# Kernel optimization log

Hardware: AMD Instinct MI355X
Metric: run time of the kernel (lower is better)

Reference implementation:

```python
import jax, jax.numpy as jnp
import numpy as np
import math

D_MODEL, N_HEADS, D_K, D_C, D_HR = 1024, 8, 128, 32, 32
B, S = 4, 2048


def setup_inputs() -> dict:
    key = jax.random.key(0)
    ks = jax.random.split(key, 17)
    def lin(k, fan_in, fan_out):
        lim = 1.0 / math.sqrt(fan_in)
        kw, kb = jax.random.split(k)
        W = jax.random.uniform(kw, (fan_in, fan_out), jnp.float32, -lim, lim)
        b = jax.random.uniform(kb, (fan_out,), jnp.float32, -lim, lim)
        return W, b
    W_DQ, b_DQ = lin(ks[0], D_MODEL, D_C)
    W_UQ, b_UQ = lin(ks[1], D_C, N_HEADS * D_K)
    W_DKV, b_DKV = lin(ks[2], D_MODEL, D_C)
    W_UK, b_UK = lin(ks[3], D_C, N_HEADS * D_K)
    W_UV, b_UV = lin(ks[4], D_C, N_HEADS * D_K)
    W_QR, b_QR = lin(ks[5], D_C, N_HEADS * D_HR)
    W_KR, b_KR = lin(ks[6], D_MODEL, D_HR)
    W_O, b_O = lin(ks[7], N_HEADS * D_K, D_MODEL)
    h_t = jax.random.normal(ks[8], (B, S, D_MODEL), jnp.float32)
    return {"h_t": h_t,
            "W_DQ": W_DQ, "b_DQ": b_DQ, "W_UQ": W_UQ, "b_UQ": b_UQ,
            "W_DKV": W_DKV, "b_DKV": b_DKV, "W_UK": W_UK, "b_UK": b_UK,
            "W_UV": W_UV, "b_UV": b_UV, "W_QR": W_QR, "b_QR": b_QR,
            "W_KR": W_KR, "b_KR": b_KR, "W_O": W_O, "b_O": b_O}


def reference(h_t, W_DQ, b_DQ, W_UQ, b_UQ, W_DKV, b_DKV, W_UK, b_UK,
              W_UV, b_UV, W_QR, b_QR, W_KR, b_KR, W_O, b_O):
    b, s, _ = h_t.shape
    # low-rank latent projections
    c_q = h_t @ W_DQ + b_DQ                       # [B,S,d_c]
    c_kv = h_t @ W_DKV + b_DKV                    # [B,S,d_c]
    # content heads: [B,H,S,d_k]
    q_c = (c_q @ W_UQ + b_UQ).reshape(b, s, N_HEADS, D_K).transpose(0, 2, 1, 3)
    k_c = (c_kv @ W_UK + b_UK).reshape(b, s, N_HEADS, D_K).transpose(0, 2, 1, 3)
    v_c = (c_kv @ W_UV + b_UV).reshape(b, s, N_HEADS, D_K).transpose(0, 2, 1, 3)
    # rope sub-dims (apply_rope is identity in the source): [B,H,S,d_hR]
    q_r = (c_q @ W_QR + b_QR).reshape(b, s, N_HEADS, D_HR).transpose(0, 2, 1, 3)
    k_r = (h_t @ W_KR + b_KR)[:, None, :, :]      # [B,1,S,d_hR], shared across heads
    k_r = jnp.broadcast_to(k_r, (b, N_HEADS, s, D_HR))
    # concat content + rope dims
    q = jnp.concatenate([q_c, q_r], axis=-1)      # [B,H,S,d_k+d_hR]
    k = jnp.concatenate([k_c, k_r], axis=-1)
    scale = 1.0 / math.sqrt(D_K + D_HR)
    scores = jnp.einsum('bhsd,bhtd->bhst', q, k) * scale
    attn = jax.nn.softmax(scores, axis=-1)
    o = jnp.einsum('bhst,bhtd->bhsd', attn, v_c)  # [B,H,S,d_k]
    o = o.transpose(0, 2, 1, 3).reshape(b, s, N_HEADS * D_K)
    return o @ W_O + b_O
```

## Files before the change

kernel.cpp:

```cpp
#include <hip/hip_runtime.h>
#include <hip/hip_bf16.h>

#define B_SZ 4
#define S_SZ 2048
#define DM   1024
#define NH   8
#define DK   128
#define DC   32
#define DHR  32
#define DQK  160
#define T_TOK (B_SZ * S_SZ)
#define SCALE 0.07905694150420949f
#define C2LOG 0.11405506439f
#define NT    (S_SZ / 64)
#define NCOL  3328

typedef unsigned int uint;
typedef unsigned short ushort;
typedef __attribute__((ext_vector_type(8))) short short8;
typedef __attribute__((ext_vector_type(4))) float floatx4;
typedef __attribute__((ext_vector_type(16))) float floatx16;
typedef __attribute__((ext_vector_type(4))) uint uintx4;

__device__ __forceinline__ ushort f2bf(float f) {
    uint u = __float_as_uint(f);
    uint r = u + 0x7fffu + ((u >> 16) & 1u);
    return (ushort)(r >> 16);
}
__device__ __forceinline__ uint packbf(float x, float y) {
    return (uint)f2bf(x) | ((uint)f2bf(y) << 16);
}

__device__ __forceinline__ void glds16(const ushort* g, ushort* l) {
    __builtin_amdgcn_global_load_lds(
        (const __attribute__((address_space(1))) uint*)g,
        (__attribute__((address_space(3))) uint*)l, 16, 0, 0);
}

__global__ __launch_bounds__(256) void prep_kernel(
    const float* __restrict__ W_O,
    const float* __restrict__ W_UQ, const float* __restrict__ b_UQ,
    const float* __restrict__ W_QR, const float* __restrict__ b_QR,
    const float* __restrict__ W_UK, const float* __restrict__ b_UK,
    const float* __restrict__ W_UV, const float* __restrict__ b_UV,
    const float* __restrict__ W_DQ, const float* __restrict__ b_DQ,
    const float* __restrict__ W_DKV, const float* __restrict__ b_DKV,
    const float* __restrict__ W_KR, const float* __restrict__ b_KR,
    ushort* __restrict__ wot,
    ushort* __restrict__ wcat, float* __restrict__ bcat,
    ushort* __restrict__ wdcat, float* __restrict__ bdcat)
{
    __shared__ float t[32][33];
    const int bid = blockIdx.x;
    const int tx = threadIdx.x & 31, ty = threadIdx.x >> 5;

    if (bid < 1024) {
        const int n0 = (bid & 31) * 32, k0 = (bid >> 5) * 32;
        #pragma unroll
        for (int j = 0; j < 32; j += 8)
            t[ty + j][tx] = W_O[(size_t)(k0 + ty + j) * DM + n0 + tx];
        __syncthreads();
        #pragma unroll
        for (int j = 0; j < 32; j += 8)
            wot[(size_t)(n0 + ty + j) * DM + k0 + tx] = f2bf(t[tx][ty + j]);
    } else if (bid < 1128) {
        const int c0 = (bid - 1024) * 32;
        const float* W; const float* bias; int stride, sc0;
        if (c0 < 1024)      { W = W_UQ; bias = b_UQ; stride = 1024; sc0 = c0; }
        else if (c0 < 1280) { W = W_QR; bias = b_QR; stride = 256;  sc0 = c0 - 1024; }
        else if (c0 < 2304) { W = W_UK; bias = b_UK; stride = 1024; sc0 = c0 - 1280; }
        else                { W = W_UV; bias = b_UV; stride = 1024; sc0 = c0 - 2304; }
        #pragma unroll
        for (int j = 0; j < 4; ++j) {
            int k = ty + j * 8;
            t[k][tx] = W[(size_t)k * stride + sc0 + tx];
        }
        __syncthreads();
        #pragma unroll
        for (int j = 0; j < 4; ++j) {
            int cc = ty + j * 8;
            wcat[(size_t)(c0 + cc) * 32 + tx] = f2bf(t[tx][cc]);
        }
        if (threadIdx.x < 32) bcat[c0 + threadIdx.x] = bias[sc0 + threadIdx.x];
    } else {
        const int idx = bid - 1128;
        const int wsel = idx >> 5;
        const int k0 = (idx & 31) * 32;
        const float* W    = (wsel == 0) ? W_DQ  : (wsel == 1) ? W_DKV : W_KR;
        const float* bias = (wsel == 0) ? b_DQ  : (wsel == 1) ? b_DKV : b_KR;
        #pragma unroll
        for (int j = 0; j < 32; j += 8)
            t[ty + j][tx] = W[(size_t)(k0 + ty + j) * 32 + tx];
        __syncthreads();
        #pragma unroll
        for (int j = 0; j < 32; j += 8)
            wdcat[(size_t)(wsel * 32 + ty + j) * DM + k0 + tx] = f2bf(t[tx][ty + j]);
        if (k0 == 0 && threadIdx.x < 32)
            bdcat[wsel * 32 + threadIdx.x] = bias[threadIdx.x];
    }
}

__global__ __launch_bounds__(128) void latent_mfma_kernel(
    const float* __restrict__ h_t,
    const ushort* __restrict__ wdcat, const float* __restrict__ bdcat,
    ushort* __restrict__ cqbf, ushort* __restrict__ ckvbf, ushort* __restrict__ krbf)
{
    const int tid  = threadIdx.x;
    const int wave = tid >> 6;
    const int lane = tid & 63;
    const int quad = lane >> 4;
    const int l16  = lane & 15;

    const int tok = blockIdx.x * 32 + wave * 16 + l16;

    floatx4 acc[6];
    #pragma unroll
    for (int ct = 0; ct < 6; ++ct) acc[ct] = (floatx4){0.f, 0.f, 0.f, 0.f};

    const float* hrow = h_t + (size_t)tok * DM + quad * 8;

    #pragma unroll 2
    for (int k0 = 0; k0 < DM; k0 += 32) {
        float4 f0 = *(const float4*)&hrow[k0];
        float4 f1 = *(const float4*)&hrow[k0 + 4];
        uint b0, b1, b2, b3;
        asm("v_cvt_pk_bf16_f32 %0, %1, %2" : "=v"(b0) : "v"(f0.x), "v"(f0.y));
        asm("v_cvt_pk_bf16_f32 %0, %1, %2" : "=v"(b1) : "v"(f0.z), "v"(f0.w));
        asm("v_cvt_pk_bf16_f32 %0, %1, %2" : "=v"(b2) : "v"(f1.x), "v"(f1.y));
        asm("v_cvt_pk_bf16_f32 %0, %1, %2" : "=v"(b3) : "v"(f1.z), "v"(f1.w));
        short8 bf = __builtin_bit_cast(short8, (uintx4){b0, b1, b2, b3});
        #pragma unroll
        for (int ct = 0; ct < 6; ++ct) {
            short8 af = *(const short8*)&wdcat[(size_t)(ct * 16 + l16) * DM + k0 + quad * 8];
            acc[ct] = __builtin_amdgcn_mfma_f32_16x16x32_bf16(af, bf, acc[ct], 0, 0, 0);
        }
    }

    const int q4 = quad * 4;
    #pragma unroll
    for (int ct = 0; ct < 6; ++ct) {
        float4 b4 = *(const float4*)&bdcat[ct * 16 + q4];
        uint w0, w1;
        asm("v_cvt_pk_bf16_f32 %0, %1, %2" : "=v"(w0)
            : "v"(acc[ct][0] + b4.x), "v"(acc[ct][1] + b4.y));
        asm("v_cvt_pk_bf16_f32 %0, %1, %2" : "=v"(w1)
            : "v"(acc[ct][2] + b4.z), "v"(acc[ct][3] + b4.w));
        int col = ct * 16 + q4;
        ushort* outp = (col < 32) ? cqbf : (col < 64) ? ckvbf : krbf;
        int cc = col & 31;
        *(uint2*)&outp[(size_t)tok * 32 + cc] = make_uint2(w0, w1);
    }
}

__global__ __launch_bounds__(256) void build_qkv_mfma_kernel(
    const ushort* __restrict__ cqbf, const ushort* __restrict__ ckvbf,
    const ushort* __restrict__ krbf,
    const ushort* __restrict__ wcat, const float* __restrict__ bcat,
    ushort* __restrict__ q_ws, ushort* __restrict__ k_ws, ushort* __restrict__ v_ws)
{
    const int tid  = threadIdx.x;
    const int wave = tid >> 6;
    const int lane = tid & 63;
    const int quad = lane >> 4;
    const int l16  = lane & 15;

    const int tok = blockIdx.x * 64 + wave * 16 + l16;
    const int hp  = blockIdx.y;
    const int bb  = tok >> 11, s = tok & 2047;

    const short8 bq  = *(const short8*)&cqbf[tok * 32 + quad * 8];
    const short8 bkv = *(const short8*)&ckvbf[tok * 32 + quad * 8];
    const uint4  kr  = *(const uint4*)&((const uint*)krbf)[tok * 16 + quad * 4];

    const int q4 = quad * 4;

    auto emit = [&](int wrow, ushort* outp, int dbase, short8 bfrag) {
        short8 af = *(const short8*)&wcat[(size_t)(wrow + l16) * 32 + quad * 8];
        floatx4 d = __builtin_amdgcn_mfma_f32_16x16x32_bf16(
            af, bfrag, (floatx4){0.f, 0.f, 0.f, 0.f}, 0, 0, 0);
        float4 b4 = *(const float4*)&bcat[wrow + q4];
        uint w0, w1;
        asm("v_cvt_pk_bf16_f32 %0, %1, %2" : "=v"(w0)
            : "v"(d[0] + b4.x), "v"(d[1] + b4.y));
        asm("v_cvt_pk_bf16_f32 %0, %1, %2" : "=v"(w1)
            : "v"(d[2] + b4.z), "v"(d[3] + b4.w));
        *(uint2*)&outp[dbase + q4] = make_uint2(w0, w1);
    };

    #pragma unroll
    for (int hh = 0; hh < 2; ++hh) {
        const int h = hp * 2 + hh;
        ushort* qp = q_ws + ((size_t)(bb * NH + h) * S_SZ + s) * DQK;
        ushort* kp = k_ws + ((size_t)(bb * NH + h) * S_SZ + s) * DQK;
        ushort* vp = v_ws + ((size_t)(bb * NH + h) * S_SZ + s) * DK;

        #pragma unroll
        for (int seg = 0; seg < 8; ++seg) emit(h * 128 + seg * 16, qp, seg * 16, bq);
        #pragma unroll
        for (int seg = 0; seg < 2; ++seg) emit(1024 + h * 32 + seg * 16, qp, 128 + seg * 16, bq);
        #pragma unroll
        for (int seg = 0; seg < 8; ++seg) emit(1280 + h * 128 + seg * 16, kp, seg * 16, bkv);
        #pragma unroll
        for (int seg = 0; seg < 8; ++seg) emit(2304 + h * 128 + seg * 16, vp, seg * 16, bkv);

        *(uint4*)&kp[128 + quad * 8] = kr;
    }
}

__global__ __launch_bounds__(256, 2) void attn_mfma_kernel(
    const ushort* __restrict__ q_ws, const ushort* __restrict__ k_ws,
    const ushort* __restrict__ v_ws, ushort* __restrict__ o_ws)
{
    __shared__ __align__(16) ushort SH[38912];
    const int tid  = threadIdx.x;
    const int wave = tid >> 6;
    const int lane = tid & 63;
    const int l32  = lane & 31;
    const int hi   = lane >> 5;
    const int hi8  = hi * 8;

    const int wg = blockIdx.x;
    const int virt = (wg & 7) * 64 + (wg >> 3);
    const int bh = virt >> 4;
    const int b = bh >> 3, h = bh & 7;
    const int s0 = (virt & 15) * 128;
    const int qrow_base = s0 + wave * 32;

    const ushort* kbase = k_ws + (size_t)bh * S_SZ * DQK;
    const ushort* vbase = v_ws + (size_t)bh * S_SZ * DK;

    int ksrc[5];
    #pragma unroll
    for (int j = 0; j < 5; ++j) {
        int d = (tid + j * 256) * 16;
        int r0 = d / 320;
        int la = d;
        #pragma unroll
        for (int dr = -1; dr <= 1; ++dr) {
            int r = r0 + dr;
            int cand = d ^ ((r & 7) << 4);
            if (cand / 320 == r) la = cand;
        }
        ksrc[j] = la;
    }
    const int kdst_us = (wave * 64) * 8;

    short8 qf[10];
    {
        const ushort* qp = q_ws + ((size_t)bh * S_SZ + qrow_base + l32) * DQK + hi8;
        #pragma unroll
        for (int st = 0; st < 10; ++st)
            qf[st] = *(const short8*)&qp[st * 16];
    }

    floatx16 oa[4];
    #pragma unroll
    for (int vt = 0; vt < 4; ++vt)
        oa[vt] = (floatx16){0.f,0.f,0.f,0.f,0.f,0.f,0.f,0.f,
                            0.f,0.f,0.f,0.f,0.f,0.f,0.f,0.f};

    float m2 = -3.0e38f;
    float l_run = 0.f;

    {
        #pragma unroll
        for (int j = 0; j < 5; ++j)
            glds16((const ushort*)((const char*)kbase + ksrc[j]),
                   SH + kdst_us + j * 2048);
        uint vpa[8], vpb[8];
        const uint* vg = (const uint*)vbase;
        #pragma unroll
        for (int c = 0; c < 8; ++c) {
            int kp = wave * 8 + c;
            vpa[c] = vg[(2 * kp) * 64 + lane];
            vpb[c] = vg[(2 * kp + 1) * 64 + lane];
        }
        uint* vt32 = (uint*)(SH + 20480);
        uint lo[8], hh[8];
        #pragma unroll
        for (int c = 0; c < 8; ++c) {
            lo[c] = (vpa[c] & 0xffffu) | (vpb[c] << 16);
            hh[c] = (vpa[c] >> 16) | (vpb[c] & 0xffff0000u);
        }
        *(uint4*)&vt32[(2 * lane) * 36 + wave * 8]     = make_uint4(lo[0], lo[1], lo[4], lo[5]);
        *(uint4*)&vt32[(2 * lane) * 36 + wave * 8 + 4] = make_uint4(lo[2], lo[3], lo[6], lo[7]);
        *(uint4*)&vt32[(2 * lane + 1) * 36 + wave * 8]     = make_uint4(hh[0], hh[1], hh[4], hh[5]);
        *(uint4*)&vt32[(2 * lane + 1) * 36 + wave * 8 + 4] = make_uint4(hh[2], hh[3], hh[6], hh[7]);
    }

    const int kmask = (l32 & 7) << 4;

    for (int kt = 0; kt < NT; ++kt) {
        const int cur = kt & 1, nxt = cur ^ 1;
        __syncthreads();

        uint vpa[8], vpb[8];
        if (kt + 1 < NT) {
            const char* kg = (const char*)(kbase + (size_t)(kt + 1) * 64 * DQK);
            #pragma unroll
            for (int j = 0; j < 5; ++j)
                glds16((const ushort*)(kg + ksrc[j]),
                       SH + nxt * 10240 + kdst_us + j * 2048);
            const uint* vg = (const uint*)(vbase + (size_t)(kt + 1) * 64 * DK);
            #pragma unroll
            for (int c = 0; c < 8; ++c) {
                int kp = wave * 8 + c;
                vpa[c] = vg[(2 * kp) * 64 + lane];
                vpb[c] = vg[(2 * kp + 1) * 64 + lane];
            }
        }

        const char* kbufc = (const char*)(SH + cur * 10240);
        floatx16 sc[2];
        __builtin_amdgcn_s_setprio(1);
        #pragma unroll
        for (int kb = 0; kb < 2; ++kb) {
            floatx16 acc = (floatx16){0.f,0.f,0.f,0.f,0.f,0.f,0.f,0.f,
                                      0.f,0.f,0.f,0.f,0.f,0.f,0.f,0.f};
            const int row_la = (kb * 32 + l32) * 320 + hi * 16;
            #pragma unroll
            for (int st = 0; st < 10; ++st) {
                short8 kf = *(const short8*)(kbufc + ((row_la + st * 32) ^ kmask));
                acc = __builtin_amdgcn_mfma_f32_32x32x16_bf16(kf, qf[st], acc, 0, 0, 0);
            }
            sc[kb] = acc;
        }
        __builtin_amdgcn_s_setprio(0);

        {
            float tmax = -3.0e38f;
            #pragma unroll
            for (int kb = 0; kb < 2; ++kb)
                #pragma unroll
                for (int r = 0; r < 16; ++r)
                    tmax = fmaxf(tmax, sc[kb][r]);
            tmax *= C2LOG;
            tmax = fmaxf(tmax, __shfl_xor(tmax, 32));

            if (__any(tmax > m2 + 8.0f)) {
                float mnew = fmaxf(m2, tmax);
                float al = __builtin_amdgcn_exp2f(m2 - mnew);
                m2 = mnew;
                l_run *= al;
                #pragma unroll
                for (int vt = 0; vt < 4; ++vt)
                    #pragma unroll
                    for (int r = 0; r < 16; ++r)
                        oa[vt][r] *= al;
            }

            float rsum = 0.f;
            #pragma unroll
            for (int kb = 0; kb < 2; ++kb)
                #pragma unroll
                for (int r = 0; r < 16; ++r) {
                    float p = __builtin_amdgcn_exp2f(__builtin_fmaf(sc[kb][r], C2LOG, -m2));
                    sc[kb][r] = p;
                    rsum += p;
                }
            rsum += __shfl_xor(rsum, 32);
            l_run += rsum;
        }

        const ushort* vtc = SH + 20480 + cur * 9216;
        __builtin_amdgcn_s_setprio(1);
        #pragma unroll
        for (int kb = 0; kb < 2; ++kb) {
            #pragma unroll
            for (int s = 0; s < 2; ++s) {
                uint w0, w1, w2, w3;
                asm("v_cvt_pk_bf16_f32 %0, %1, %2" : "=v"(w0)
                    : "v"(sc[kb][8 * s + 0]), "v"(sc[kb][8 * s + 1]));
                asm("v_cvt_pk_bf16_f32 %0, %1, %2" : "=v"(w1)
                    : "v"(sc[kb][8 * s + 2]), "v"(sc[kb][8 * s + 3]));
                asm("v_cvt_pk_bf16_f32 %0, %1, %2" : "=v"(w2)
                    : "v"(sc[kb][8 * s + 4]), "v"(sc[kb][8 * s + 5]));
                asm("v_cvt_pk_bf16_f32 %0, %1, %2" : "=v"(w3)
                    : "v"(sc[kb][8 * s + 6]), "v"(sc[kb][8 * s + 7]));
                short8 pv = __builtin_bit_cast(short8, (uintx4){w0, w1, w2, w3});
                #pragma unroll
                for (int vt = 0; vt < 4; ++vt) {
                    short8 vf = *(const short8*)&vtc[(size_t)(vt * 32 + l32) * 72
                                                     + kb * 32 + s * 16 + hi8];
                    oa[vt] = __builtin_amdgcn_mfma_f32_32x32x16_bf16(vf, pv, oa[vt], 0, 0, 0);
                }
            }
        }
        __builtin_amdgcn_s_setprio(0);

        if (kt + 1 < NT) {
            uint* vt32 = (uint*)(SH + 20480 + nxt * 9216);
            uint lo[8], hh[8];
            #pragma unroll
            for (int c = 0; c < 8; ++c) {
                lo[c] = (vpa[c] & 0xffffu) | (vpb[c] << 16);
                hh[c] = (vpa[c] >> 16) | (vpb[c] & 0xffff0000u);
            }
            *(uint4*)&vt32[(2 * lane) * 36 + wave * 8]     = make_uint4(lo[0], lo[1], lo[4], lo[5]);
            *(uint4*)&vt32[(2 * lane) * 36 + wave * 8 + 4] = make_uint4(lo[2], lo[3], lo[6], lo[7]);
            *(uint4*)&vt32[(2 * lane + 1) * 36 + wave * 8]     = make_uint4(hh[0], hh[1], hh[4], hh[5]);
            *(uint4*)&vt32[(2 * lane + 1) * 36 + wave * 8 + 4] = make_uint4(hh[2], hh[3], hh[6], hh[7]);
        }
    }

    __syncthreads();
    ushort* ot = SH + wave * (32 * 136);
    uint* ot32 = (uint*)ot;
    {
        float inv = 1.0f / l_run;
        #pragma unroll
        for (int vt = 0; vt < 4; ++vt)
            #pragma unroll
            for (int g = 0; g < 4; ++g) {
                int base = l32 * 68 + vt * 16 + g * 4 + hi * 2;
                ot32[base]     = packbf(oa[vt][g * 4 + 0] * inv, oa[vt][g * 4 + 1] * inv);
                ot32[base + 1] = packbf(oa[vt][g * 4 + 2] * inv, oa[vt][g * 4 + 3] * inv);
            }
    }
    #pragma unroll
    for (int pass = 0; pass < 8; ++pass) {
        int row_in = pass * 4 + (lane >> 4);
        int col8 = (lane & 15) * 8;
        uint4 v = *(const uint4*)&ot[row_in * 136 + col8];
        int srow = qrow_base + row_in;
        *(uint4*)(o_ws + (((size_t)b * S_SZ + srow) * NH + h) * DK + col8) = v;
    }
}

__global__ __launch_bounds__(256) void out_gemm_mfma_kernel(
    const ushort* __restrict__ A,
    const ushort* __restrict__ BT,
    const float* __restrict__ b_O, float* __restrict__ out)
{
    __shared__ __align__(16) ushort As[128 * 32];
    __shared__ __align__(16) ushort Bs[128 * 32];

    const int tid = threadIdx.x;
    const int wave = tid >> 6;
    const int lane = tid & 63;
    const int quad = lane >> 4;
    const int l16 = lane & 15;
    const int wr = wave >> 1, wc = wave & 1;

    const int n0 = blockIdx.x * 128;
    const int m0 = blockIdx.y * 128;

    const int lrow = lane >> 2;
    const int lseg = (lane & 3) * 8;

    floatx4 acc[4][4];
    #pragma unroll
    for (int mt = 0; mt < 4; ++mt)
        #pragma unroll
        for (int nt = 0; nt < 4; ++nt)
            acc[mt][nt] = (floatx4){0.f, 0.f, 0.f, 0.f};

    for (int k0 = 0; k0 < DM; k0 += 32) {
        __syncthreads();
        {
            const ushort* g0 = A + (size_t)(m0 + wave * 32 + lrow) * DM + k0 + lseg;
            glds16(g0, &As[(wave * 32) * 32]);
            const ushort* g1 = A + (size_t)(m0 + wave * 32 + 16 + lrow) * DM + k0 + lseg;
            glds16(g1, &As[(wave * 32 + 16) * 32]);
        }
        {
            const ushort* g0 = BT + (size_t)(n0 + wave * 32 + lrow) * DM + k0 + lseg;
            glds16(g0, &Bs[(wave * 32) * 32]);
            const ushort* g1 = BT + (size_t)(n0 + wave * 32 + 16 + lrow) * DM + k0 + lseg;
            glds16(g1, &Bs[(wave * 32 + 16) * 32]);
        }
        __syncthreads();

        short8 af[4], bf[4];
        #pragma unroll
        for (int mt = 0; mt < 4; ++mt)
            af[mt] = *(const short8*)&As[(wr * 64 + mt * 16 + l16) * 32 + quad * 8];
        #pragma unroll
        for (int nt = 0; nt < 4; ++nt)
            bf[nt] = *(const short8*)&Bs[(wc * 64 + nt * 16 + l16) * 32 + quad * 8];
        #pragma unroll
        for (int mt = 0; mt < 4; ++mt)
            #pragma unroll
            for (int nt = 0; nt < 4; ++nt)
                acc[mt][nt] = __builtin_amdgcn_mfma_f32_16x16x32_bf16(af[mt], bf[nt], acc[mt][nt], 0, 0, 0);
    }

    float bo[4];
    #pragma unroll
    for (int nt = 0; nt < 4; ++nt) bo[nt] = b_O[n0 + wc * 64 + nt * 16 + l16];

    #pragma unroll
    for (int mt = 0; mt < 4; ++mt) {
        #pragma unroll
        for (int r = 0; r < 4; ++r) {
            int row = m0 + wr * 64 + mt * 16 + quad * 4 + r;
            float* orow = out + (size_t)row * DM + n0 + wc * 64;
            #pragma unroll
            for (int nt = 0; nt < 4; ++nt)
                orow[nt * 16 + l16] = acc[mt][nt][r] + bo[nt];
        }
    }
}

extern "C" void kernel_launch(void* const* d_in, const int* in_sizes, int n_in,
                              void* d_out, int out_size, void* d_ws, size_t ws_size,
                              hipStream_t stream) {
    (void)in_sizes; (void)n_in; (void)out_size; (void)ws_size;

    const float* h_t   = (const float*)d_in[0];
    const float* W_DQ  = (const float*)d_in[1];
    const float* b_DQ  = (const float*)d_in[2];
    const float* W_UQ  = (const float*)d_in[3];
    const float* b_UQ  = (const float*)d_in[4];
    const float* W_DKV = (const float*)d_in[5];
    const float* b_DKV = (const float*)d_in[6];
    const float* W_UK  = (const float*)d_in[7];
    const float* b_UK  = (const float*)d_in[8];
    const float* W_UV  = (const float*)d_in[9];
    const float* b_UV  = (const float*)d_in[10];
    const float* W_QR  = (const float*)d_in[11];
    const float* b_QR  = (const float*)d_in[12];
    const float* W_KR  = (const float*)d_in[13];
    const float* b_KR  = (const float*)d_in[14];
    const float* W_O   = (const float*)d_in[15];
    const float* b_O   = (const float*)d_in[16];

    ushort* cqbf  = (ushort*)d_ws;
    ushort* ckvbf = cqbf + (size_t)T_TOK * DC;
    ushort* krbf  = ckvbf + (size_t)T_TOK * DC;
    ushort* wcat  = krbf + (size_t)T_TOK * DC;
    float*  bcat  = (float*)(wcat + (size_t)NCOL * DC);
    ushort* wdcat = (ushort*)(bcat + NCOL);
    float*  bdcat = (float*)(wdcat + (size_t)96 * DM);
    ushort* q_ws  = (ushort*)(bdcat + 96);
    ushort* k_ws  = q_ws + (size_t)B_SZ * NH * S_SZ * DQK;
    ushort* v_ws  = k_ws + (size_t)B_SZ * NH * S_SZ * DQK;
    ushort* o_ws  = v_ws + (size_t)B_SZ * NH * S_SZ * DK;
    ushort* wot   = o_ws + (size_t)T_TOK * DM;

    float* out = (float*)d_out;

    prep_kernel<<<1224, 256, 0, stream>>>(
        W_O, W_UQ, b_UQ, W_QR, b_QR, W_UK, b_UK, W_UV, b_UV,
        W_DQ, b_DQ, W_DKV, b_DKV, W_KR, b_KR,
        wot, wcat, bcat, wdcat, bdcat);

    latent_mfma_kernel<<<T_TOK / 32, 128, 0, stream>>>(
        h_t, wdcat, bdcat, cqbf, ckvbf, krbf);

    build_qkv_mfma_kernel<<<dim3(T_TOK / 64, 4), 256, 0, stream>>>(
        cqbf, ckvbf, krbf, wcat, bcat, q_ws, k_ws, v_ws);

    attn_mfma_kernel<<<512, 256, 0, stream>>>(
        q_ws, k_ws, v_ws, o_ws);

    out_gemm_mfma_kernel<<<dim3(DM / 128, T_TOK / 128), 256, 0, stream>>>(
        o_ws, wot, b_O, out);
}
```

Before: 270.9 us.

## Stage latent-projection inputs through swizzled LDS and widen output GEMM K-tile

New measurement: 271.4 us. No clear change (+0.2%).

```diff
diff --git a/kernel.cpp b/kernel.cpp
--- a/kernel.cpp
+++ b/kernel.cpp
@@ -105,50 +105,78 @@
     const ushort* __restrict__ wdcat, const float* __restrict__ bdcat,
     ushort* __restrict__ cqbf, ushort* __restrict__ ckvbf, ushort* __restrict__ krbf)
 {
+    __shared__ __align__(16) float hsl[2 * 2048];
     const int tid  = threadIdx.x;
     const int wave = tid >> 6;
     const int lane = tid & 63;
     const int quad = lane >> 4;
     const int l16  = lane & 15;
-
-    const int tok = blockIdx.x * 32 + wave * 16 + l16;
-
-    floatx4 acc[6];
-    #pragma unroll
-    for (int ct = 0; ct < 6; ++ct) acc[ct] = (floatx4){0.f, 0.f, 0.f, 0.f};
-
-    const float* hrow = h_t + (size_t)tok * DM + quad * 8;
-
-    #pragma unroll 2
-    for (int k0 = 0; k0 < DM; k0 += 32) {
-        float4 f0 = *(const float4*)&hrow[k0];
-        float4 f1 = *(const float4*)&hrow[k0 + 4];
-        uint b0, b1, b2, b3;
-        asm("v_cvt_pk_bf16_f32 %0, %1, %2" : "=v"(b0) : "v"(f0.x), "v"(f0.y));
-        asm("v_cvt_pk_bf16_f32 %0, %1, %2" : "=v"(b1) : "v"(f0.z), "v"(f0.w));
-        asm("v_cvt_pk_bf16_f32 %0, %1, %2" : "=v"(b2) : "v"(f1.x), "v"(f1.y));
-        asm("v_cvt_pk_bf16_f32 %0, %1, %2" : "=v"(b3) : "v"(f1.z), "v"(f1.w));
-        short8 bf = __builtin_bit_cast(short8, (uintx4){b0, b1, b2, b3});
-        #pragma unroll
-        for (int ct = 0; ct < 6; ++ct) {
-            short8 af = *(const short8*)&wdcat[(size_t)(ct * 16 + l16) * DM + k0 + quad * 8];
-            acc[ct] = __builtin_amdgcn_mfma_f32_16x16x32_bf16(af, bf, acc[ct], 0, 0, 0);
+    const int t0 = blockIdx.x * 16;
+
+    int soff[4], ldst[4];
+    #pragma unroll
+    for (int j = 0; j < 4; ++j) {
+        int d = (tid + j * 128) * 16;
+        int la = d ^ (((d >> 9) & 7) << 4);
+        soff[j] = (d >> 9) * 4096 + (la & 511);
+        ldst[j] = (wave * 64 + j * 128) * 16;
+    }
+    const char* hbase = (const char*)(h_t + (size_t)t0 * DM);
+
+    #pragma unroll
+    for (int j = 0; j < 4; ++j)
+        glds16((const ushort*)(hbase + soff[j]), (ushort*)((char*)hsl + ldst[j]));
+
+    floatx4 acc[3];
+    #pragma unroll
+    for (int ct = 0; ct < 3; ++ct) acc[ct] = (floatx4){0.f, 0.f, 0.f, 0.f};
+
+    const int xorm = (l16 & 7) << 4;
+
+    for (int c = 0; c < 8; ++c) {
+        const int cur = c & 1, nxt = cur ^ 1;
+        __syncthreads();
+        if (c + 1 < 8) {
+            #pragma unroll
+            for (int j = 0; j < 4; ++j)
+                glds16((const ushort*)(hbase + (c + 1) * 512 + soff[j]),
+                       (ushort*)((char*)hsl + nxt * 8192 + ldst[j]));
+        }
+        const char* hb = (const char*)hsl + cur * 8192;
+        #pragma unroll
+        for (int st = 0; st < 4; ++st) {
+            const int la0 = l16 * 512 + st * 128 + quad * 32;
+            float4 f0 = *(const float4*)(hb + (la0 ^ xorm));
+            float4 f1 = *(const float4*)(hb + ((la0 + 16) ^ xorm));
+            uint b0, b1, b2, b3;
+            asm("v_cvt_pk_bf16_f32 %0, %1, %2" : "=v"(b0) : "v"(f0.x), "v"(f0.y));
+            asm("v_cvt_pk_bf16_f32 %0, %1, %2" : "=v"(b1) : "v"(f0.z), "v"(f0.w));
+            asm("v_cvt_pk_bf16_f32 %0, %1, %2" : "=v"(b2) : "v"(f1.x), "v"(f1.y));
+            asm("v_cvt_pk_bf16_f32 %0, %1, %2" : "=v"(b3) : "v"(f1.z), "v"(f1.w));
+            short8 bfr = __builtin_bit_cast(short8, (uintx4){b0, b1, b2, b3});
+            #pragma unroll
+            for (int ct = 0; ct < 3; ++ct) {
+                const int wct = wave * 3 + ct;
+                short8 af = *(const short8*)&wdcat[(size_t)(wct * 16 + l16) * DM
+                                                   + c * 128 + st * 32 + quad * 8];
+                acc[ct] = __builtin_amdgcn_mfma_f32_16x16x32_bf16(af, bfr, acc[ct], 0, 0, 0);
+            }
         }
     }
 
     const int q4 = quad * 4;
-    #pragma unroll
-    for (int ct = 0; ct < 6; ++ct) {
-        float4 b4 = *(const float4*)&bdcat[ct * 16 + q4];
+    const int tok = t0 + l16;
+    #pragma unroll
+    for (int ct = 0; ct < 3; ++ct) {
+        const int col = (wave * 3 + ct) * 16 + q4;
+        float4 b4 = *(const float4*)&bdcat[col];
         uint w0, w1;
         asm("v_cvt_pk_bf16_f32 %0, %1, %2" : "=v"(w0)
             : "v"(acc[ct][0] + b4.x), "v"(acc[ct][1] + b4.y));
         asm("v_cvt_pk_bf16_f32 %0, %1, %2" : "=v"(w1)
             : "v"(acc[ct][2] + b4.z), "v"(acc[ct][3] + b4.w));
-        int col = ct * 16 + q4;
         ushort* outp = (col < 32) ? cqbf : (col < 64) ? ckvbf : krbf;
-        int cc = col & 31;
-        *(uint2*)&outp[(size_t)tok * 32 + cc] = make_uint2(w0, w1);
+        *(uint2*)&outp[(size_t)tok * 32 + (col & 31)] = make_uint2(w0, w1);
     }
 }
 
@@ -432,8 +460,8 @@
     const ushort* __restrict__ BT,
     const float* __restrict__ b_O, float* __restrict__ out)
 {
-    __shared__ __align__(16) ushort As[128 * 32];
-    __shared__ __align__(16) ushort Bs[128 * 32];
+    __shared__ __align__(16) ushort As[128 * 64];
+    __shared__ __align__(16) ushort Bs[128 * 64];
 
     const int tid = threadIdx.x;
     const int wave = tid >> 6;
@@ -442,11 +470,19 @@
     const int l16 = lane & 15;
     const int wr = wave >> 1, wc = wave & 1;
 
-    const int n0 = blockIdx.x * 128;
-    const int m0 = blockIdx.y * 128;
-
-    const int lrow = lane >> 2;
-    const int lseg = (lane & 3) * 8;
+    const int wg = blockIdx.x;
+    const int virt = (wg & 7) * 64 + (wg >> 3);
+    const int n0 = (virt & 7) * 128;
+    const int m0 = (virt >> 3) * 128;
+
+    int soff[4], ldst[4];
+    #pragma unroll
+    for (int j = 0; j < 4; ++j) {
+        int d = (tid + j * 256) * 16;
+        int la = d ^ (((d >> 7) & 7) << 4);
+        soff[j] = (d >> 7) * 2048 + (la & 127);
+        ldst[j] = (wave * 64 + j * 256) * 16;
+    }
 
     floatx4 acc[4][4];
     #pragma unroll
@@ -455,34 +491,36 @@
         for (int nt = 0; nt < 4; ++nt)
             acc[mt][nt] = (floatx4){0.f, 0.f, 0.f, 0.f};
 
-    for (int k0 = 0; k0 < DM; k0 += 32) {
-        __syncthreads();
-        {
-            const ushort* g0 = A + (size_t)(m0 + wave * 32 + lrow) * DM + k0 + lseg;
-            glds16(g0, &As[(wave * 32) * 32]);
-            const ushort* g1 = A + (size_t)(m0 + wave * 32 + 16 + lrow) * DM + k0 + lseg;
-            glds16(g1, &As[(wave * 32 + 16) * 32]);
-        }
-        {
-            const ushort* g0 = BT + (size_t)(n0 + wave * 32 + lrow) * DM + k0 + lseg;
-            glds16(g0, &Bs[(wave * 32) * 32]);
-            const ushort* g1 = BT + (size_t)(n0 + wave * 32 + 16 + lrow) * DM + k0 + lseg;
-            glds16(g1, &Bs[(wave * 32 + 16) * 32]);
-        }
-        __syncthreads();
-
-        short8 af[4], bf[4];
+    const int xorm = (l16 & 7) << 4;
+
+    for (int k0 = 0; k0 < DM; k0 += 64) {
+        __syncthreads();
+        #pragma unroll
+        for (int j = 0; j < 4; ++j) {
+            glds16((const ushort*)((const char*)A + (size_t)m0 * 2048 + k0 * 2 + soff[j]),
+                   (ushort*)((char*)As + ldst[j]));
+            glds16((const ushort*)((const char*)BT + (size_t)n0 * 2048 + k0 * 2 + soff[j]),
+                   (ushort*)((char*)Bs + ldst[j]));
+        }
+        __syncthreads();
+
+        short8 af[4][2], bf[4][2];
         #pragma unroll
         for (int mt = 0; mt < 4; ++mt)
-            af[mt] = *(const short8*)&As[(wr * 64 + mt * 16 + l16) * 32 + quad * 8];
-        #pragma unroll
-        for (int nt = 0; nt < 4; ++nt)
-            bf[nt] = *(const short8*)&Bs[(wc * 64 + nt * 16 + l16) * 32 + quad * 8];
+            #pragma unroll
+            for (int hh = 0; hh < 2; ++hh) {
+                int la_a = (wr * 64 + mt * 16 + l16) * 128 + hh * 64 + quad * 16;
+                af[mt][hh] = *(const short8*)((const char*)As + (la_a ^ xorm));
+                int la_b = (wc * 64 + mt * 16 + l16) * 128 + hh * 64 + quad * 16;
+                bf[mt][hh] = *(const short8*)((const char*)Bs + (la_b ^ xorm));
+            }
         #pragma unroll
         for (int mt = 0; mt < 4; ++mt)
             #pragma unroll
-            for (int nt = 0; nt < 4; ++nt)
-                acc[mt][nt] = __builtin_amdgcn_mfma_f32_16x16x32_bf16(af[mt], bf[nt], acc[mt][nt], 0, 0, 0);
+            for (int nt = 0; nt < 4; ++nt) {
+                acc[mt][nt] = __builtin_amdgcn_mfma_f32_16x16x32_bf16(af[mt][0], bf[nt][0], acc[mt][nt], 0, 0, 0);
+                acc[mt][nt] = __builtin_amdgcn_mfma_f32_16x16x32_bf16(af[mt][1], bf[nt][1], acc[mt][nt], 0, 0, 0);
+            }
     }
 
     float bo[4];
@@ -545,7 +583,7 @@
         W_DQ, b_DQ, W_DKV, b_DKV, W_KR, b_KR,
         wot, wcat, bcat, wdcat, bdcat);
 
-    latent_mfma_kernel<<<T_TOK / 32, 128, 0, stream>>>(
+    latent_mfma_kernel<<<T_TOK / 16, 128, 0, stream>>>(
         h_t, wdcat, bdcat, cqbf, ckvbf, krbf);
 
     build_qkv_mfma_kernel<<<dim3(T_TOK / 64, 4), 256, 0, stream>>>(
@@ -554,6 +592,6 @@
     attn_mfma_kernel<<<512, 256, 0, stream>>>(
         q_ws, k_ws, v_ws, o_ws);
 
-    out_gemm_mfma_kernel<<<dim3(DM / 128, T_TOK / 128), 256, 0, stream>>>(
+    out_gemm_mfma_kernel<<<512, 256, 0, stream>>>(
         o_ws, wot, b_O, out);
 }
```
